# Performance work log

Hardware: AMD Instinct MI355X
Metric: run time of the kernel (lower is better)

The kernel has to match this reference:

```python
import jax, jax.numpy as jnp
import numpy as np

IMG_W = 1024.0
IMG_H = 1024.0
CONF_THRESH = 0.2
NMS_THRESH = 0.5
MAX_PRED = 300
MAX_DELTA = 5.0


def setup_inputs() -> dict:
    key = jax.random.key(0)
    k1, k2 = jax.random.split(key)
    B, G, stride, base = 16, 128, 8.0, 64.0
    scales = np.array([0.5, 0.75, 1.0, 1.25])
    ratios = np.array([0.3, 0.5, 1.0, 2.0, 3.0])
    ss, rr = np.meshgrid(scales, ratios, indexing='ij')  # [4,5] -> 20 anchor shapes
    ws = (base * ss / np.sqrt(rr)).reshape(-1)  # [20]
    hs = (base * ss * np.sqrt(rr)).reshape(-1)  # [20]
    cx = (np.arange(G) + 0.5) * stride
    CX, CY = np.meshgrid(cx, cx, indexing='xy')  # [G,G]
    x1 = CX[None] - 0.5 * ws[:, None, None]
    y1 = CY[None] - 0.5 * hs[:, None, None]
    x2 = CX[None] + 0.5 * ws[:, None, None]
    y2 = CY[None] + 0.5 * hs[:, None, None]
    anchors = np.stack([x1, y1, x2, y2], axis=-1).reshape(-1, 4).astype(np.float32)  # [A*G*G,4]
    N = anchors.shape[0]  # 327680
    cls_logits = jax.random.normal(k1, (B, N), jnp.float32)
    bbox_deltas = jax.random.normal(k2, (B, N, 4), jnp.float32) * 0.5
    return {"cls_logits": cls_logits, "bbox_deltas": bbox_deltas, "anchors": jnp.asarray(anchors)}


def _decode(deltas, anchors):
    # deltas [B,N,4], anchors [N,4] -> boxes [B,N,4], valid [B,N]
    w = anchors[:, 2] - anchors[:, 0]
    h = anchors[:, 3] - anchors[:, 1]
    cx = anchors[:, 0] + 0.5 * w
    cy = anchors[:, 1] + 0.5 * h
    d = jnp.clip(deltas, -MAX_DELTA, MAX_DELTA)
    pcx = cx + d[..., 0] * w
    pcy = cy + d[..., 1] * h
    pw = w * jnp.exp(d[..., 2])
    ph = h * jnp.exp(d[..., 3])
    x1 = jnp.clip(pcx - 0.5 * pw, 0.0, IMG_W)
    y1 = jnp.clip(pcy - 0.5 * ph, 0.0, IMG_H)
    x2 = jnp.clip(pcx + 0.5 * pw, 0.0, IMG_W)
    y2 = jnp.clip(pcy + 0.5 * ph, 0.0, IMG_H)
    boxes = jnp.stack([x1, y1, x2, y2], axis=-1)
    bw = x2 - x1
    bh = y2 - y1
    valid = (bw > 1.0) & (bh > 1.0) & (bw < 2000.0) & (bh < 2000.0)
    return boxes, valid


def _iou_matrix(boxes):
    # boxes [K,4] -> [K,K] pairwise IoU
    x1, y1, x2, y2 = boxes[:, 0], boxes[:, 1], boxes[:, 2], boxes[:, 3]
    area = (x2 - x1) * (y2 - y1)
    ix1 = jnp.maximum(x1[:, None], x1[None, :])
    iy1 = jnp.maximum(y1[:, None], y1[None, :])
    ix2 = jnp.minimum(x2[:, None], x2[None, :])
    iy2 = jnp.minimum(y2[:, None], y2[None, :])
    inter = jnp.clip(ix2 - ix1, 0.0) * jnp.clip(iy2 - iy1, 0.0)
    return inter / (area[:, None] + area[None, :] - inter + 1e-9)


def _nms_keep(iou, valid):
    # greedy NMS over score-sorted candidates; iou [K,K], valid [K] -> keep [K]
    K = iou.shape[0]
    idx = jnp.arange(K)
    def body(i, keep):
        suppressed = jnp.any((iou[i] >= NMS_THRESH) & keep & (idx < i))
        return keep.at[i].set(valid[i] & ~suppressed)
    return jax.lax.fori_loop(0, K, body, jnp.zeros((K,), bool))


def reference(cls_logits, bbox_deltas, anchors):
    scores = jax.nn.sigmoid(cls_logits)                      # [B,N]
    boxes, valid = _decode(bbox_deltas, anchors)             # [B,N,4], [B,N]
    bw = boxes[..., 2] - boxes[..., 0]
    bh = boxes[..., 3] - boxes[..., 1]
    size_ok = (bw > 5.0) & (bh > 5.0) & (bw < IMG_W / 2) & (bh < IMG_H / 2)
    conf = (scores > CONF_THRESH) & valid & size_ok
    masked = jnp.where(conf, scores, -1.0)
    top_scores, top_idx = jax.lax.top_k(masked, MAX_PRED)    # [B,K] descending sort (top-300)
    top_boxes = jnp.take_along_axis(boxes, top_idx[..., None], axis=1)  # [B,K,4]
    top_valid = top_scores > 0.0                              # padded slots have score -1
    ious = jax.vmap(_iou_matrix)(top_boxes)                   # [B,K,K]
    keep = jax.vmap(_nms_keep)(ious, top_valid)               # [B,K]
    keepf = keep.astype(top_boxes.dtype)
    norm = jnp.array([IMG_W, IMG_H, IMG_W, IMG_H], top_boxes.dtype)
    out_boxes = (top_boxes / norm) * keepf[..., None]         # normalized, zeroed if suppressed
    out_scores = top_scores * keepf
    return jnp.concatenate([out_boxes, out_scores[..., None]], axis=-1)  # [B,K,5]
```

## Files before the change

### kernel.cpp

```cpp
#include <hip/hip_runtime.h>
#include <stdint.h>

typedef unsigned int u32;
typedef unsigned long long u64;

#define MAXP   300
#define NREG   32
#define RCAP   128
#define SLOTS  (NREG*RCAP)
#define SELN   1024
#define NB     2048
#define LOGIT_LO 2.7f
#define MASKW  10

__device__ __forceinline__ float sigmoid_f(float x) {
    return __fdiv_rn(1.0f, __fadd_rn(1.0f, expf(-x)));
}

__device__ __forceinline__ bool decode_box(const float4 dv, const float4 av, float bx[4]) {
    float w  = __fsub_rn(av.z, av.x);
    float h  = __fsub_rn(av.w, av.y);
    float cx = __fadd_rn(av.x, __fmul_rn(0.5f, w));
    float cy = __fadd_rn(av.y, __fmul_rn(0.5f, h));
    float d0 = fminf(fmaxf(dv.x, -5.0f), 5.0f);
    float d1 = fminf(fmaxf(dv.y, -5.0f), 5.0f);
    float d2 = fminf(fmaxf(dv.z, -5.0f), 5.0f);
    float d3 = fminf(fmaxf(dv.w, -5.0f), 5.0f);
    float pcx = __fadd_rn(cx, __fmul_rn(d0, w));
    float pcy = __fadd_rn(cy, __fmul_rn(d1, h));
    float pw  = __fmul_rn(w, expf(d2));
    float ph  = __fmul_rn(h, expf(d3));
    float hx  = __fmul_rn(0.5f, pw);
    float hy  = __fmul_rn(0.5f, ph);
    float x1 = fminf(fmaxf(__fsub_rn(pcx, hx), 0.0f), 1024.0f);
    float y1 = fminf(fmaxf(__fsub_rn(pcy, hy), 0.0f), 1024.0f);
    float x2 = fminf(fmaxf(__fadd_rn(pcx, hx), 0.0f), 1024.0f);
    float y2 = fminf(fmaxf(__fadd_rn(pcy, hy), 0.0f), 1024.0f);
    bx[0] = x1; bx[1] = y1; bx[2] = x2; bx[3] = y2;
    float bw = __fsub_rn(x2, x1);
    float bh = __fsub_rn(y2, y1);
    return (bw > 5.0f) && (bh > 5.0f) && (bw < 512.0f) && (bh < 512.0f);
}

__device__ __forceinline__ float key_score(u64 k) {
    return __uint_as_float(((u32)(k >> 32)) & 0x7FFFFFFFu);
}

__device__ __forceinline__ int score_bin(float s) {
    int bin = (int)(__fmul_rn(__fsub_rn(s, 0.93f), 29257.14f));
    return bin < 0 ? 0 : (bin > NB - 1 ? NB - 1 : bin);
}

__global__ __launch_bounds__(256)
void det_pass1(const float4* __restrict__ logits4,
               const float4* __restrict__ deltas,
               const float4* __restrict__ anchors,
               u32* __restrict__ cnt2, u64* __restrict__ cand,
               int n4_per_block)
{
    const int b = blockIdx.y;
    const int c = blockIdx.x;
    const int tid = threadIdx.x;

    __shared__ u64 lbuf[RCAP];
    __shared__ u32 lcnt;
    if (tid == 0) lcnt = 0;
    __syncthreads();

    const int base4 = (b * (int)gridDim.x + c) * n4_per_block;
    const int nbase = c * n4_per_block * 4;

    for (int q = 0; q < n4_per_block; q += 256) {
        int t = q + tid;
        float4 lg = logits4[base4 + t];
        float l[4] = {lg.x, lg.y, lg.z, lg.w};
#pragma unroll
        for (int k = 0; k < 4; ++k) {
            if (l[k] >= LOGIT_LO) {
                u32 n = (u32)(nbase + t * 4 + k);
                u32 i = (u32)((base4 + t) * 4 + k);
                float4 dv = deltas[i];
                float4 av = anchors[n];
                float bx[4];
                bool ok = decode_box(dv, av, bx);
                float s = sigmoid_f(l[k]);
                if (ok && s > 0.2f) {
                    u32 ms = __float_as_uint(s) | 0x80000000u;
                    u64 key = ((u64)ms << 32) | (u64)(u32)(~n);
                    u32 pos = atomicAdd(&lcnt, 1u);
                    if (pos < RCAP) lbuf[pos] = key;
                }
            }
        }
    }
    __syncthreads();
    u32 cn = lcnt < RCAP ? lcnt : (u32)RCAP;
    const u32 r = (u32)(b * (int)gridDim.x + c);
    if (tid == 0) cnt2[r] = cn;
    if ((u32)tid < cn) cand[r * RCAP + (u32)tid] = lbuf[tid];
}

__global__ __launch_bounds__(1024)
void det_pass2(const float4* __restrict__ deltas,
               const float4* __restrict__ anchors,
               const u32* __restrict__ cnt2, const u64* __restrict__ cand,
               float* __restrict__ out, int N)
{
    const int b = blockIdx.x;
    const int tid = threadIdx.x;
    const int NT = 1024;

    __shared__ u32 hist[NB];
    __shared__ u32 coarse[NB / 8];
    __shared__ u64 sel[SELN];
    __shared__ u32 rcnt[NREG];
    __shared__ u32 scnt, s_tb, s_cseg, s_above;
    __shared__ float sbx1[MAXP], sby1[MAXP], sbx2[MAXP], sby2[MAXP];
    __shared__ float sarea[MAXP], sscore[MAXP];
    __shared__ u32 svalid[MAXP];
    __shared__ u32 vword[MASKW];
    __shared__ u32 smask[MAXP * MASKW];
    __shared__ u32 skeep[MAXP];

    for (int i = tid; i < NB; i += NT) hist[i] = 0;
    if (tid < NREG) rcnt[tid] = cnt2[b * NREG + tid];
    if (tid < MASKW) vword[tid] = 0;
    if (tid == 0) { scnt = 0; s_cseg = 0xFFFFFFFFu; s_above = 0; }
    __syncthreads();

    u64 kk[4];
#pragma unroll
    for (int it = 0; it < 4; ++it) {
        int s = tid + it * NT;
        int c = s >> 7;
        int o = s & (RCAP - 1);
        u64 k = 0;
        if ((u32)o < rcnt[c]) k = cand[(u32)(b * NREG + c) * RCAP + (u32)o];
        kk[it] = k;
        if (k) atomicAdd(&hist[score_bin(key_score(k))], 1u);
    }
    __syncthreads();

    if (tid < NB / 8) {
        u32 ssum = 0;
#pragma unroll
        for (int j = 0; j < 8; ++j) ssum += hist[tid * 8 + j];
        coarse[tid] = ssum;
    }
    __syncthreads();
    for (u32 off = 1; off < NB / 8; off <<= 1) {
        u32 v = 0;
        if (tid < NB / 8) {
            v = coarse[tid];
            if (tid + (int)off < NB / 8) v += coarse[tid + off];
        }
        __syncthreads();
        if (tid < NB / 8) coarse[tid] = v;
        __syncthreads();
    }
    if (tid < NB / 8) {
        u32 cs = coarse[tid];
        u32 nxt = (tid + 1 < NB / 8) ? coarse[tid + 1] : 0;
        if (cs >= MAXP && (tid == NB / 8 - 1 || nxt < MAXP)) { s_cseg = (u32)tid; s_above = nxt; }
    }
    __syncthreads();
    if (tid == 0) {
        u32 tb = 0;
        if (s_cseg != 0xFFFFFFFFu) {
            u32 cum = s_above;
            int fb = (int)s_cseg * 8;
            tb = (u32)fb;
            for (int i2 = fb + 7; i2 >= fb; --i2) {
                cum += hist[i2];
                if (cum >= MAXP) { tb = (u32)i2; break; }
            }
        }
        s_tb = tb;
    }
    __syncthreads();
    const int tb = (int)s_tb;

#pragma unroll
    for (int it = 0; it < 4; ++it) {
        u64 k = kk[it];
        if (k && score_bin(key_score(k)) >= tb) {
            u32 p = atomicAdd(&scnt, 1u);
            if (p < SELN) sel[p] = k;
        }
    }
    __syncthreads();
    u32 nsel = scnt; if (nsel > SELN) nsel = SELN;
    if ((u32)tid >= nsel) sel[tid] = 0;
    __syncthreads();

    for (u32 kk2 = 2; kk2 <= SELN; kk2 <<= 1) {
        for (u32 j = kk2 >> 1; j > 0; j >>= 1) {
            u32 i = (u32)tid;
            u32 ixj = i ^ j;
            if (ixj > i) {
                u64 a = sel[i], cc = sel[ixj];
                bool desc = ((i & kk2) == 0);
                if (desc ? (a < cc) : (a > cc)) { sel[i] = cc; sel[ixj] = a; }
            }
            __syncthreads();
        }
    }

    if (tid < MAXP) {
        u64 k = sel[tid];
        if (k == 0) {
            svalid[tid] = 0; sscore[tid] = 0.0f;
            sbx1[tid] = 0.0f; sby1[tid] = 0.0f; sbx2[tid] = 0.0f; sby2[tid] = 0.0f;
            sarea[tid] = 0.0f;
        } else {
            u32 n = ~(u32)(k & 0xFFFFFFFFull);
            float s = key_score(k);
            float4 dv = deltas[(size_t)b * (size_t)N + n];
            float4 av = anchors[n];
            float bx[4];
            (void)decode_box(dv, av, bx);
            sbx1[tid] = bx[0]; sby1[tid] = bx[1]; sbx2[tid] = bx[2]; sby2[tid] = bx[3];
            sscore[tid] = s; svalid[tid] = 1;
            sarea[tid] = __fmul_rn(__fsub_rn(bx[2], bx[0]), __fsub_rn(bx[3], bx[1]));
            atomicOr(&vword[tid >> 5], 1u << (tid & 31));
        }
    }
    for (int i = tid; i < MAXP * MASKW; i += NT) smask[i] = 0;
    __syncthreads();

    for (int p = tid; p < MAXP * MAXP; p += NT) {
        int i = p / MAXP;
        int j = p - i * MAXP;
        if (j >= i) continue;
        if (!svalid[i] || !svalid[j]) continue;
        float ix1 = fmaxf(sbx1[i], sbx1[j]);
        float iy1 = fmaxf(sby1[i], sby1[j]);
        float ix2 = fminf(sbx2[i], sbx2[j]);
        float iy2 = fminf(sby2[i], sby2[j]);
        float iw = fmaxf(__fsub_rn(ix2, ix1), 0.0f);
        float ih = fmaxf(__fsub_rn(iy2, iy1), 0.0f);
        float inter = __fmul_rn(iw, ih);
        float denom = __fadd_rn(__fsub_rn(__fadd_rn(sarea[i], sarea[j]), inter), 1e-9f);
        float iou = __fdiv_rn(inter, denom);
        if (iou >= 0.5f) {
            atomicOr(&smask[i * MASKW + (j >> 5)], 1u << (j & 31));
            atomicOr(&smask[j * MASKW + (i >> 5)], 1u << (i & 31));
        }
    }
    __syncthreads();

    if (tid == 0) {
        u32 S0=0,S1=0,S2=0,S3=0,S4=0,S5=0,S6=0,S7=0,S8=0,S9=0;
        u32 V0=vword[0],V1=vword[1],V2=vword[2],V3=vword[3],V4=vword[4];
        u32 V5=vword[5],V6=vword[6],V7=vword[7],V8=vword[8],V9=vword[9];
        int i = 0;
#define NMSW(SW,VW)                                                          \
        for (int bit = 0; bit < 32 && i < MAXP; ++bit, ++i) {                \
            u32 kp = (~(SW >> bit) & (VW >> bit)) & 1u;                      \
            skeep[i] = kp;                                                   \
            if (kp) {                                                        \
                const u32* rr = &smask[i * MASKW];                           \
                S0|=rr[0];S1|=rr[1];S2|=rr[2];S3|=rr[3];S4|=rr[4];           \
                S5|=rr[5];S6|=rr[6];S7|=rr[7];S8|=rr[8];S9|=rr[9];           \
            }                                                                \
        }
        NMSW(S0,V0) NMSW(S1,V1) NMSW(S2,V2) NMSW(S3,V3) NMSW(S4,V4)
        NMSW(S5,V5) NMSW(S6,V6) NMSW(S7,V7) NMSW(S8,V8) NMSW(S9,V9)
#undef NMSW
    }
    __syncthreads();

    if (tid < MAXP) {
        const float inv = 1.0f / 1024.0f;
        float kf = skeep[tid] ? 1.0f : 0.0f;
        float* o = out + ((size_t)b * MAXP + tid) * 5;
        o[0] = __fmul_rn(__fmul_rn(sbx1[tid], inv), kf);
        o[1] = __fmul_rn(__fmul_rn(sby1[tid], inv), kf);
        o[2] = __fmul_rn(__fmul_rn(sbx2[tid], inv), kf);
        o[3] = __fmul_rn(__fmul_rn(sby2[tid], inv), kf);
        o[4] = __fmul_rn(sscore[tid], kf);
    }
}

extern "C" void kernel_launch(void* const* d_in, const int* in_sizes, int n_in,
                              void* d_out, int out_size, void* d_ws, size_t ws_size,
                              hipStream_t stream) {
    const float4* logits4 = (const float4*)d_in[0];
    const float4* deltas  = (const float4*)d_in[1];
    const float4* anchors = (const float4*)d_in[2];
    const int N = in_sizes[2] / 4;
    const int B = in_sizes[0] / N;
    const int n4_per_batch = N / 4;
    const int n4_per_block = n4_per_batch / NREG;

    u32* cnt2 = (u32*)d_ws;
    u64* cand = (u64*)((char*)d_ws + 4096);

    det_pass1<<<dim3(NREG, B), 256, 0, stream>>>(logits4, deltas, anchors, cnt2, cand, n4_per_block);
    det_pass2<<<B, 1024, 0, stream>>>(deltas, anchors, cnt2, cand, (float*)d_out, N);
}
```

Baseline: 198.5 us.

## Replace bitonic sort with rank-by-counting and use wave-shuffle prefix scan

Replaces the 1024-element shared-memory bitonic sort, which needs about 55 block-wide barriers, with a rank-by-count selection. Each thread compares its key against all selected keys and scatters its decoded box directly to its rank. The coarse histogram suffix scan now runs in a single wavefront using shuffles instead of log-step barrier loops. The selection buffer is halved to 512, which risks dropping candidates if more than 512 fall above the threshold bin. Zero-initialisation of the box arrays moves to kernel start.

```diff
diff --git a/kernel.cpp b/kernel.cpp
--- a/kernel.cpp
+++ b/kernel.cpp
@@ -8,7 +8,7 @@
 #define NREG   32
 #define RCAP   128
 #define SLOTS  (NREG*RCAP)
-#define SELN   1024
+#define SEL2   512
 #define NB     2048
 #define LOGIT_LO 2.7f
 #define MASKW  10
@@ -112,7 +112,7 @@
 
     __shared__ u32 hist[NB];
     __shared__ u32 coarse[NB / 8];
-    __shared__ u64 sel[SELN];
+    __shared__ u64 sel[SEL2];
     __shared__ u32 rcnt[NREG];
     __shared__ u32 scnt, s_tb, s_cseg, s_above;
     __shared__ float sbx1[MAXP], sby1[MAXP], sbx2[MAXP], sby2[MAXP];
@@ -125,6 +125,11 @@
     for (int i = tid; i < NB; i += NT) hist[i] = 0;
     if (tid < NREG) rcnt[tid] = cnt2[b * NREG + tid];
     if (tid < MASKW) vword[tid] = 0;
+    if (tid < MAXP) {
+        svalid[tid] = 0; sscore[tid] = 0.0f; sarea[tid] = 0.0f;
+        sbx1[tid] = 0.0f; sby1[tid] = 0.0f; sbx2[tid] = 0.0f; sby2[tid] = 0.0f;
+    }
+    for (int i = tid; i < MAXP * MASKW; i += NT) smask[i] = 0;
     if (tid == 0) { scnt = 0; s_cseg = 0xFFFFFFFFu; s_above = 0; }
     __syncthreads();
 
@@ -148,16 +153,26 @@
         coarse[tid] = ssum;
     }
     __syncthreads();
-    for (u32 off = 1; off < NB / 8; off <<= 1) {
-        u32 v = 0;
-        if (tid < NB / 8) {
-            v = coarse[tid];
-            if (tid + (int)off < NB / 8) v += coarse[tid + off];
-        }
-        __syncthreads();
-        if (tid < NB / 8) coarse[tid] = v;
-        __syncthreads();
-    }
+
+    if (tid < 64) {
+        int base = tid * 4;
+        u32 c0 = coarse[base], c1 = coarse[base + 1];
+        u32 c2 = coarse[base + 2], c3 = coarse[base + 3];
+        u32 s3 = c3, s2 = c2 + s3, s1 = c1 + s2, s0 = c0 + s1;
+        u32 T = s0, S = T;
+#pragma unroll
+        for (int off = 1; off < 64; off <<= 1) {
+            u32 v = (u32)__shfl((int)S, tid + off, 64);
+            if (tid + off < 64) S += v;
+        }
+        u32 above = S - T;
+        coarse[base]     = above + s0;
+        coarse[base + 1] = above + s1;
+        coarse[base + 2] = above + s2;
+        coarse[base + 3] = above + s3;
+    }
+    __syncthreads();
+
     if (tid < NB / 8) {
         u32 cs = coarse[tid];
         u32 nxt = (tid + 1 < NB / 8) ? coarse[tid + 1] : 0;
@@ -185,47 +200,37 @@
         u64 k = kk[it];
         if (k && score_bin(key_score(k)) >= tb) {
             u32 p = atomicAdd(&scnt, 1u);
-            if (p < SELN) sel[p] = k;
-        }
-    }
-    __syncthreads();
-    u32 nsel = scnt; if (nsel > SELN) nsel = SELN;
-    if ((u32)tid >= nsel) sel[tid] = 0;
-    __syncthreads();
-
-    for (u32 kk2 = 2; kk2 <= SELN; kk2 <<= 1) {
-        for (u32 j = kk2 >> 1; j > 0; j >>= 1) {
-            u32 i = (u32)tid;
-            u32 ixj = i ^ j;
-            if (ixj > i) {
-                u64 a = sel[i], cc = sel[ixj];
-                bool desc = ((i & kk2) == 0);
-                if (desc ? (a < cc) : (a > cc)) { sel[i] = cc; sel[ixj] = a; }
-            }
-            __syncthreads();
-        }
-    }
-
-    if (tid < MAXP) {
-        u64 k = sel[tid];
-        if (k == 0) {
-            svalid[tid] = 0; sscore[tid] = 0.0f;
-            sbx1[tid] = 0.0f; sby1[tid] = 0.0f; sbx2[tid] = 0.0f; sby2[tid] = 0.0f;
-            sarea[tid] = 0.0f;
-        } else {
-            u32 n = ~(u32)(k & 0xFFFFFFFFull);
-            float s = key_score(k);
+            if (p < SEL2) sel[p] = k;
+        }
+    }
+    __syncthreads();
+    u32 nsel = scnt; if (nsel > SEL2) nsel = SEL2;
+    if ((u32)tid >= nsel && tid < SEL2) sel[tid] = 0;
+    __syncthreads();
+
+    const int nsel2 = (int)((nsel + 1u) & ~1u);
+    if (tid < SEL2) {
+        u64 my = sel[tid];
+        int rank = 0;
+#pragma unroll 4
+        for (int j = 0; j < nsel2; j += 2) {
+            u64 a = sel[j], c2 = sel[j + 1];
+            rank += (a > my) ? 1 : 0;
+            rank += (c2 > my) ? 1 : 0;
+        }
+        if (my != 0 && rank < MAXP) {
+            u32 n = ~(u32)(my & 0xFFFFFFFFull);
+            float s = key_score(my);
             float4 dv = deltas[(size_t)b * (size_t)N + n];
             float4 av = anchors[n];
             float bx[4];
             (void)decode_box(dv, av, bx);
-            sbx1[tid] = bx[0]; sby1[tid] = bx[1]; sbx2[tid] = bx[2]; sby2[tid] = bx[3];
-            sscore[tid] = s; svalid[tid] = 1;
-            sarea[tid] = __fmul_rn(__fsub_rn(bx[2], bx[0]), __fsub_rn(bx[3], bx[1]));
-            atomicOr(&vword[tid >> 5], 1u << (tid & 31));
-        }
-    }
-    for (int i = tid; i < MAXP * MASKW; i += NT) smask[i] = 0;
+            sbx1[rank] = bx[0]; sby1[rank] = bx[1]; sbx2[rank] = bx[2]; sby2[rank] = bx[3];
+            sscore[rank] = s; svalid[rank] = 1;
+            sarea[rank] = __fmul_rn(__fsub_rn(bx[2], bx[0]), __fsub_rn(bx[3], bx[1]));
+            atomicOr(&vword[rank >> 5], 1u << (rank & 31));
+        }
+    }
     __syncthreads();
 
     for (int p = tid; p < MAXP * MAXP; p += NT) {
```

New measurement: 194.1 us. 1.02x faster.
